# Kernel optimization log

Hardware: AMD Instinct MI355X
Metric: run time of the kernel (lower is better)

The kernel has to match this reference:

```python
import jax, jax.numpy as jnp
import numpy as np

EPS = 1e-5  # torch LayerNorm default

def layernorm(x, gamma, beta):
    mu = jnp.mean(x, axis=-1, keepdims=True)
    var = jnp.mean(jnp.square(x - mu), axis=-1, keepdims=True)
    return (x - mu) * jax.lax.rsqrt(var + EPS) * gamma + beta

def setup_inputs() -> dict:
    key = jax.random.key(0)
    ks = jax.random.split(key, 8)
    B, S, D = 4, 2048, 1024
    s = 1.0 / np.sqrt(D)  # torch Linear init scale
    return {
        "x": jax.random.normal(ks[0], (B, S, D), dtype=jnp.float32),
        "Wq": jax.random.uniform(ks[1], (D, D), jnp.float32, -s, s),
        "bq": jax.random.uniform(ks[2], (D,), jnp.float32, -s, s),
        "Wk": jax.random.uniform(ks[3], (D, D), jnp.float32, -s, s),
        "bk": jax.random.uniform(ks[4], (D,), jnp.float32, -s, s),
        "Wv": jax.random.uniform(ks[5], (D, D), jnp.float32, -s, s),
        "bv": jax.random.uniform(ks[6], (D,), jnp.float32, -s, s),
        "gamma": jnp.ones((D,), jnp.float32),
        "beta": jnp.zeros((D,), jnp.float32),
    }

def reference(x, Wq, bq, Wk, bk, Wv, bv, gamma, beta):
    # torch Linear: x @ W.T + b; shared LayerNorm applied to each projection
    q = layernorm(jnp.einsum('bsd,ed->bse', x, Wq) + bq, gamma, beta)
    k = layernorm(jnp.einsum('bsd,ed->bse', x, Wk) + bk, gamma, beta)
    v = layernorm(jnp.einsum('bsd,ed->bse', x, Wv) + bv, gamma, beta)
    att = jnp.einsum('bqd,bkd->bqk', q, k)  # no 1/sqrt(d) scaling in original
    att = jax.nn.softmax(att, axis=-1)
    # dropout is identity in eval mode (reference baseline)
    return jnp.einsum('bqk,bkd->bqd', att, v)
```

## Files before the change

kernel.cpp:

```cpp
#include <hip/hip_runtime.h>

typedef _Float16 f16;
typedef __attribute__((ext_vector_type(4))) _Float16 f16x4;
typedef __attribute__((ext_vector_type(8))) _Float16 f16x8;
typedef __attribute__((ext_vector_type(4))) float f32x4;

#define GLB_AS __attribute__((address_space(1)))
#define LDS_AS __attribute__((address_space(3)))

__device__ __forceinline__ void async_copy16(const void* g, void* l) {
  __builtin_amdgcn_global_load_lds((const GLB_AS void*)g, (LDS_AS void*)l, 16, 0, 0);
}

template <typename OutT, int MODE, bool BIAS>
__global__ __launch_bounds__(256) void gemm_kn(
    const f16* __restrict__ A, const f16* __restrict__ B, OutT* __restrict__ C,
    int lda, int ldb, int ldc, int K, long sA, long sB, long sC,
    int tiles_x, int tiles_y,
    const float* __restrict__ b0, const float* __restrict__ b1,
    const float* __restrict__ b2)
{
  constexpr int BM = 128, BK = 32;
  __shared__ __align__(16) f16 Ash[2][BM * BK];
  __shared__ __align__(16) f16 Bsh[2][BM * BK];

  int bx, by, bz;
  {
    const int n = blockIdx.x;
    if (MODE == 0) {
      by = n % tiles_y;
      const int r = n / tiles_y;
      bx = r % tiles_x;
      bz = r / tiles_x;
    } else {
      const int j = n & 7, i = n >> 3;
      bz = j >> 1;
      bx = i >> 3;
      by = (j & 1) * 8 + (i & 7);
    }
  }

  A += (long)bz * sA;
  B += (long)bz * sB;
  C += (long)bz * sC;

  const int tid  = threadIdx.x;
  const int wave = tid >> 6, lane = tid & 63;
  const int m0 = by * BM, n0 = bx * BM;
  const int wm = (wave >> 1) * 64, wn = (wave & 1) * 64;
  const int r16 = lane & 15, quad = lane >> 4;

  const int srow = wave * 32 + (lane >> 2);
  const int skb  = (((lane & 3) ^ ((lane >> 3) & 3))) * 8;
  const f16* Ag = A + (long)(m0 + srow) * lda + skb;
  const f16* Bg = B + (long)(n0 + srow) * ldb + skb;
  const int lo0 = (wave * 32) * BK;
  const int lo1 = (wave * 32 + 16) * BK;

  async_copy16(Ag,                  &Ash[0][lo0]);
  async_copy16(Ag + 16 * (long)lda, &Ash[0][lo1]);
  async_copy16(Bg,                  &Bsh[0][lo0]);
  async_copy16(Bg + 16 * (long)ldb, &Bsh[0][lo1]);

  f32x4 acc[4][4] = {};

  const int kidx = (quad ^ ((r16 >> 1) & 3)) * 8;

  int buf = 0;
  for (int k0 = 0; k0 < K; k0 += BK, buf ^= 1) {
    __syncthreads();

    if (k0 + BK < K) {
      const int nb = buf ^ 1;
      const long k1 = k0 + BK;
      async_copy16(Ag + k1,                  &Ash[nb][lo0]);
      async_copy16(Ag + k1 + 16 * (long)lda, &Ash[nb][lo1]);
      async_copy16(Bg + k1,                  &Bsh[nb][lo0]);
      async_copy16(Bg + k1 + 16 * (long)ldb, &Bsh[nb][lo1]);
    }

    f16x8 af[4], bf[4];
#pragma unroll
    for (int i = 0; i < 4; i++) {
      af[i] = *(const f16x8*)&Ash[buf][(wm + i * 16 + r16) * BK + kidx];
      bf[i] = *(const f16x8*)&Bsh[buf][(wn + i * 16 + r16) * BK + kidx];
    }
#pragma unroll
    for (int i = 0; i < 4; i++)
#pragma unroll
      for (int j = 0; j < 4; j++)
        acc[i][j] = __builtin_amdgcn_mfma_f32_16x16x32_f16(af[i], bf[j], acc[i][j], 0, 0, 0);
  }

  float bias_j[4] = {0.f, 0.f, 0.f, 0.f};
  if (BIAS) {
    const float* bias = (bz == 0) ? b0 : (bz == 1) ? b1 : b2;
#pragma unroll
    for (int j = 0; j < 4; j++) bias_j[j] = bias[n0 + wn + j * 16 + r16];
  }
#pragma unroll
  for (int i = 0; i < 4; i++)
#pragma unroll
    for (int j = 0; j < 4; j++)
#pragma unroll
      for (int r = 0; r < 4; r++) {
        long row = m0 + wm + i * 16 + quad * 4 + r;
        long col = n0 + wn + j * 16 + r16;
        C[row * (long)ldc + col] = (OutT)(acc[i][j][r] + bias_j[j]);
      }
}

__global__ __launch_bounds__(256) void cast_all(
    const float* __restrict__ x, const float* __restrict__ Wq,
    const float* __restrict__ Wk, const float* __restrict__ Wv,
    f16* __restrict__ Xh, f16* __restrict__ Wh)
{
  const long off = (long)blockIdx.x * 1024 + threadIdx.x * 4;
  const float* src;
  f16* dst;
  if (off < 8388608L) {
    src = x + off;
    dst = Xh + off;
  } else {
    const long o = off - 8388608L;
    src = (o < 1048576L) ? Wq + o
        : (o < 2097152L) ? Wk + (o - 1048576L)
                         : Wv + (o - 2097152L);
    dst = Wh + o;
  }
  const float4 v = *(const float4*)src;
  f16x4 h;
  h.x = (f16)v.x; h.y = (f16)v.y; h.z = (f16)v.z; h.w = (f16)v.w;
  *(f16x4*)dst = h;
}

__global__ __launch_bounds__(256) void ln_kernel(
    f16* __restrict__ P, const float* __restrict__ gamma,
    const float* __restrict__ beta)
{
  f16* p = P + (long)blockIdx.y * 8388608 + (long)blockIdx.x * 1024;
  const int tid = threadIdx.x;
  const int e = tid * 4;

  f16x4 raw = *(const f16x4*)(p + e);
  float v0 = (float)raw.x, v1 = (float)raw.y;
  float v2 = (float)raw.z, v3 = (float)raw.w;
  float s  = v0 + v1 + v2 + v3;
  float s2 = v0 * v0 + v1 * v1 + v2 * v2 + v3 * v3;

#pragma unroll
  for (int off = 32; off > 0; off >>= 1) {
    s  += __shfl_down(s, off, 64);
    s2 += __shfl_down(s2, off, 64);
  }
  __shared__ float red[10];
  const int wave = tid >> 6, lane = tid & 63;
  if (lane == 0) { red[wave] = s; red[4 + wave] = s2; }
  __syncthreads();
  if (tid == 0) {
    red[8] = red[0] + red[1] + red[2] + red[3];
    red[9] = red[4] + red[5] + red[6] + red[7];
  }
  __syncthreads();
  const float mu   = red[8] * (1.f / 1024.f);
  const float var  = red[9] * (1.f / 1024.f) - mu * mu;
  const float rstd = rsqrtf(var + 1e-5f);

  float4 gg = *(const float4*)(gamma + e);
  float4 be = *(const float4*)(beta + e);
  f16x4 o;
  o.x = (f16)((v0 - mu) * rstd * gg.x + be.x);
  o.y = (f16)((v1 - mu) * rstd * gg.y + be.y);
  o.z = (f16)((v2 - mu) * rstd * gg.z + be.z);
  o.w = (f16)((v3 - mu) * rstd * gg.w + be.w);
  *(f16x4*)(p + e) = o;
}

__global__ __launch_bounds__(256) void transpose_kernel(const f16* __restrict__ V,
                                                        f16* __restrict__ Vt)
{
  const int S = 2048, D = 1024;
  const f16* v = V + (long)blockIdx.z * ((long)S * D);
  f16* vt = Vt + (long)blockIdx.z * ((long)D * S);
  __shared__ f16 tile[64][66];
  const int d0 = blockIdx.x * 64, j0 = blockIdx.y * 64;
  const int tx = threadIdx.x & 63, ty = threadIdx.x >> 6;
#pragma unroll
  for (int r = ty; r < 64; r += 4)
    tile[r][tx] = v[(long)(j0 + r) * D + d0 + tx];
  __syncthreads();
#pragma unroll
  for (int r = ty; r < 64; r += 4)
    vt[(long)(d0 + r) * S + j0 + tx] = tile[tx][r];
}

__global__ __launch_bounds__(256) void softmax_kernel(float* __restrict__ Sc)
{
  float* srow = Sc + (long)blockIdx.x * 2048;
  const int tid = threadIdx.x;
  float4 a = ((const float4*)srow)[tid];
  float4 b = ((const float4*)srow)[256 + tid];

  float m = fmaxf(fmaxf(fmaxf(a.x, a.y), fmaxf(a.z, a.w)),
                  fmaxf(fmaxf(b.x, b.y), fmaxf(b.z, b.w)));
#pragma unroll
  for (int off = 32; off > 0; off >>= 1) m = fmaxf(m, __shfl_down(m, off, 64));
  __shared__ float red[6];
  const int wave = tid >> 6, lane = tid & 63;
  if (lane == 0) red[wave] = m;
  __syncthreads();
  if (tid == 0) red[4] = fmaxf(fmaxf(red[0], red[1]), fmaxf(red[2], red[3]));
  __syncthreads();
  const float M = red[4];

  a.x = __expf(a.x - M); a.y = __expf(a.y - M);
  a.z = __expf(a.z - M); a.w = __expf(a.w - M);
  b.x = __expf(b.x - M); b.y = __expf(b.y - M);
  b.z = __expf(b.z - M); b.w = __expf(b.w - M);
  float s = a.x + a.y + a.z + a.w + b.x + b.y + b.z + b.w;
#pragma unroll
  for (int off = 32; off > 0; off >>= 1) s += __shfl_down(s, off, 64);
  if (lane == 0) red[wave] = s;
  __syncthreads();
  if (tid == 0) red[5] = red[0] + red[1] + red[2] + red[3];
  __syncthreads();
  const float inv = 1.0f / red[5];

  f16* orow = (f16*)srow;
  f16x4 oa, ob;
  oa.x = (f16)(a.x * inv); oa.y = (f16)(a.y * inv);
  oa.z = (f16)(a.z * inv); oa.w = (f16)(a.w * inv);
  ob.x = (f16)(b.x * inv); ob.y = (f16)(b.y * inv);
  ob.z = (f16)(b.z * inv); ob.w = (f16)(b.w * inv);
  ((f16x4*)orow)[tid]       = oa;
  ((f16x4*)orow)[256 + tid] = ob;
}

extern "C" void kernel_launch(void* const* d_in, const int* in_sizes, int n_in,
                              void* d_out, int out_size, void* d_ws, size_t ws_size,
                              hipStream_t stream)
{
  const float* x     = (const float*)d_in[0];
  const float* Wq    = (const float*)d_in[1];
  const float* bq    = (const float*)d_in[2];
  const float* Wk    = (const float*)d_in[3];
  const float* bk    = (const float*)d_in[4];
  const float* Wv    = (const float*)d_in[5];
  const float* bv    = (const float*)d_in[6];
  const float* gamma = (const float*)d_in[7];
  const float* beta  = (const float*)d_in[8];
  float* out = (float*)d_out;

  char* ws = (char*)d_ws;
  f16*   P  = (f16*)(ws);
  f16*   Vt = (f16*)(ws + (48u << 20));
  float* Sc = (float*)(ws + (64u << 20));
  f16*   Xh = (f16*)(ws + (64u << 20));
  f16*   Wh = (f16*)(ws + (80u << 20));

  cast_all<<<11264, 256, 0, stream>>>(x, Wq, Wk, Wv, Xh, Wh);

  gemm_kn<f16, 0, true><<<1536, 256, 0, stream>>>(
      Xh, Wh, P, 1024, 1024, 1024, 1024, 0L, 1048576L, 8388608L,
      8, 64, bq, bk, bv);

  ln_kernel<<<dim3(8192, 3), 256, 0, stream>>>(P, gamma, beta);

  transpose_kernel<<<dim3(16, 32, 4), 256, 0, stream>>>(P + 2L * 8388608, Vt);

  gemm_kn<float, 1, false><<<1024, 256, 0, stream>>>(
      P, P + 8388608, Sc, 1024, 1024, 2048, 1024, 2097152L, 2097152L, 4194304L,
      16, 16, nullptr, nullptr, nullptr);

  softmax_kernel<<<8192, 256, 0, stream>>>(Sc);

  gemm_kn<float, 1, false><<<512, 256, 0, stream>>>(
      (const f16*)Sc, Vt, out, 4096, 2048, 1024, 2048, 8388608L, 2097152L, 2097152L,
      8, 16, nullptr, nullptr, nullptr);
}
```

Before: 311.1 us.

## Triple-buffer GEMM shared-memory tiles with explicit vmcnt waits

```diff
diff --git a/kernel.cpp b/kernel.cpp
--- a/kernel.cpp
+++ b/kernel.cpp
@@ -21,8 +21,8 @@
     const float* __restrict__ b2)
 {
   constexpr int BM = 128, BK = 32;
-  __shared__ __align__(16) f16 Ash[2][BM * BK];
-  __shared__ __align__(16) f16 Bsh[2][BM * BK];
+  __shared__ __align__(16) f16 Ash[3][BM * BK];
+  __shared__ __align__(16) f16 Bsh[3][BM * BK];
 
   int bx, by, bz;
   {
@@ -57,39 +57,45 @@
   const int lo0 = (wave * 32) * BK;
   const int lo1 = (wave * 32 + 16) * BK;
 
-  async_copy16(Ag,                  &Ash[0][lo0]);
-  async_copy16(Ag + 16 * (long)lda, &Ash[0][lo1]);
-  async_copy16(Bg,                  &Bsh[0][lo0]);
-  async_copy16(Bg + 16 * (long)ldb, &Bsh[0][lo1]);
+  auto stage = [&](int b, long kk) {
+    async_copy16(Ag + kk,                   &Ash[b][lo0]);
+    async_copy16(Ag + kk + 16 * (long)lda,  &Ash[b][lo1]);
+    async_copy16(Bg + kk,                   &Bsh[b][lo0]);
+    async_copy16(Bg + kk + 16 * (long)ldb,  &Bsh[b][lo1]);
+  };
+
+  stage(0, 0);
+  if (BK < K) stage(1, BK);
 
   f32x4 acc[4][4] = {};
 
   const int kidx = (quad ^ ((r16 >> 1) & 3)) * 8;
 
-  int buf = 0;
-  for (int k0 = 0; k0 < K; k0 += BK, buf ^= 1) {
-    __syncthreads();
-
+  int cbuf = 0;
+  for (int k0 = 0; k0 < K; k0 += BK) {
     if (k0 + BK < K) {
-      const int nb = buf ^ 1;
-      const long k1 = k0 + BK;
-      async_copy16(Ag + k1,                  &Ash[nb][lo0]);
-      async_copy16(Ag + k1 + 16 * (long)lda, &Ash[nb][lo1]);
-      async_copy16(Bg + k1,                  &Bsh[nb][lo0]);
-      async_copy16(Bg + k1 + 16 * (long)ldb, &Bsh[nb][lo1]);
+      asm volatile("s_waitcnt vmcnt(4)\n\ts_barrier" ::: "memory");
+      if (k0 + 2 * BK < K) {
+        int pbuf = cbuf + 2; if (pbuf >= 3) pbuf -= 3;
+        stage(pbuf, k0 + 2 * BK);
+      }
+    } else {
+      asm volatile("s_waitcnt vmcnt(0)\n\ts_barrier" ::: "memory");
     }
 
     f16x8 af[4], bf[4];
 #pragma unroll
     for (int i = 0; i < 4; i++) {
-      af[i] = *(const f16x8*)&Ash[buf][(wm + i * 16 + r16) * BK + kidx];
-      bf[i] = *(const f16x8*)&Bsh[buf][(wn + i * 16 + r16) * BK + kidx];
+      af[i] = *(const f16x8*)&Ash[cbuf][(wm + i * 16 + r16) * BK + kidx];
+      bf[i] = *(const f16x8*)&Bsh[cbuf][(wn + i * 16 + r16) * BK + kidx];
     }
 #pragma unroll
     for (int i = 0; i < 4; i++)
 #pragma unroll
       for (int j = 0; j < 4; j++)
         acc[i][j] = __builtin_amdgcn_mfma_f32_16x16x32_f16(af[i], bf[j], acc[i][j], 0, 0, 0);
+
+    cbuf = (cbuf == 2) ? 0 : cbuf + 1;
   }
 
   float bias_j[4] = {0.f, 0.f, 0.f, 0.f};
```

Result: no change. 312.6 us (+0.5%).
